# Kernel tuning notes

Measured on AMD Instinct MI355X. Metric: run time of the kernel, lower is better.

Reference implementation:

```python
import jax, jax.numpy as jnp
import numpy as np

B, N, T, ET = 256, 256, 100, 4
MSG_HID, MSG_OUT, N_HID, N_CLASSES = 128, 64, 64, 2
N_EDGES = N * (N - 1) // 2  # 32640


def _xavier(k, out_dim, in_dim):
    std = (2.0 / (in_dim + out_dim)) ** 0.5
    return jax.random.normal(k, (out_dim, in_dim), dtype=jnp.float32) * std


def setup_inputs() -> dict:
    key = jax.random.key(0)
    ks = jax.random.split(key, 7)
    return {
        "inputs": jax.random.normal(ks[0], (B, N, T), dtype=jnp.float32),
        "sparse_edges": jax.random.uniform(ks[1], (B, N_EDGES, ET), dtype=jnp.float32),
        "w1": _xavier(ks[2], MSG_HID, N), "b1": jnp.full((MSG_HID,), 0.1, jnp.float32),
        "w2": _xavier(ks[3], MSG_OUT, MSG_HID), "b2": jnp.full((MSG_OUT,), 0.1, jnp.float32),
        "wo1": _xavier(ks[4], N_HID, MSG_OUT), "bo1": jnp.full((N_HID,), 0.1, jnp.float32),
        "wo2": _xavier(ks[5], N_HID, N_HID), "bo2": jnp.full((N_HID,), 0.1, jnp.float32),
        "wo3": _xavier(ks[6], N_CLASSES, N_HID), "bo3": jnp.full((N_CLASSES,), 0.1, jnp.float32),
    }


def reference(inputs, sparse_edges, w1, b1, w2, b2, wo1, bo1, wo2, bo2, wo3, bo3):
    b, n, _ = inputs.shape
    r, c = np.triu_indices(n, k=1)  # static index pattern
    # Scatter all non-null edge types at once: [B, ET-1, N, N]
    se = jnp.swapaxes(sparse_edges[:, :, 1:], 1, 2)  # [B, ET-1, E]
    adj = jnp.zeros((b, se.shape[1], n, n), dtype=se.dtype)
    adj = adj.at[:, :, r, c].set(se)
    adj = adj + jnp.swapaxes(adj, -1, -2)  # symmetrize
    # Message MLP (dropout_prob = 0 -> identity)
    h = jax.nn.relu(jnp.einsum('beij,hj->beih', adj, w1) + b1)   # [B,ET-1,N,msg_hid]
    m = jax.nn.relu(jnp.einsum('beih,oh->beio', h, w2) + b2)     # [B,ET-1,N,msg_out]
    # Weighted sum over edge types: weight for type i is i*0.2, i=1..ET-1
    wts = (jnp.arange(1, sparse_edges.shape[2]) * 0.2).astype(m.dtype)
    out = jnp.einsum('beio,e->bio', m, wts)                      # [B,N,msg_out]
    # Output head
    p = jax.nn.relu(out @ wo1.T + bo1)
    p = jax.nn.relu(p @ wo2.T + bo2)
    p = jnp.mean(p, axis=1)  # mean over atoms
    return p @ wo3.T + bo3   # [B, n_classes]
```

## Files before the change

### kernel.cpp

```cpp
#include <hip/hip_runtime.h>

#define B_   256
#define N_   256
#define E_   32640
#define MH   128
#define MO   64
#define NH   64

typedef __bf16 bf16x8 __attribute__((ext_vector_type(8)));
typedef float  f32x4  __attribute__((ext_vector_type(4)));

__device__ __forceinline__ unsigned short cvt_bf16(float f) {
  unsigned u = __float_as_uint(f);
  u = (u + 0x7FFFu + ((u >> 16) & 1u)) >> 16;
  return (unsigned short)u;
}

__device__ __forceinline__ bf16x8 ldfrag(const unsigned short* base, int row, int kbyte, int rowbytes) {
  int byte = (row * rowbytes + kbyte) ^ ((row & 7) << 4);
  return *reinterpret_cast<const bf16x8*>(reinterpret_cast<const char*>(base) + byte);
}

__device__ __forceinline__ void st2(unsigned short* base, int row, int colbyte, int rowbytes, unsigned short v) {
  int byte = (row * rowbytes + colbyte) ^ ((row & 7) << 4);
  *reinterpret_cast<unsigned short*>(reinterpret_cast<char*>(base) + byte) = v;
}

__device__ __forceinline__ void stage_w(unsigned short* dst, const float* __restrict__ src,
                                        int elems, int lcols, int tid) {
  for (int t = tid; t < (elems >> 2); t += 512) {
    int idx = t << 2;
    const float4 v = *reinterpret_cast<const float4*>(src + idx);
    int row = idx >> lcols;
    ushort4 u = make_ushort4(cvt_bf16(v.x), cvt_bf16(v.y), cvt_bf16(v.z), cvt_bf16(v.w));
    int byte = (idx * 2) ^ ((row & 7) << 4);
    *reinterpret_cast<ushort4*>(reinterpret_cast<char*>(dst) + byte) = u;
  }
}

__global__ __launch_bounds__(512, 2) void mlpdec_kernel(
    const float* __restrict__ se_g,
    const float* __restrict__ w1,  const float* __restrict__ b1,
    const float* __restrict__ w2,  const float* __restrict__ b2,
    const float* __restrict__ wo1, const float* __restrict__ bo1,
    const float* __restrict__ wo2, const float* __restrict__ bo2,
    const float* __restrict__ wo3, const float* __restrict__ bo3,
    float* __restrict__ out)
{
  __shared__ __align__(16) unsigned short sW1[MH * N_];
  __shared__ __align__(16) unsigned short sW2[MO * MH];
  __shared__ __align__(16) unsigned short sWO1[NH * MO];
  __shared__ __align__(16) unsigned short sWO2[NH * NH];
  __shared__ __align__(16) unsigned short sA[3][32 * N_];
  __shared__ __align__(16) unsigned short sHXP[32 * MH];
  __shared__ float sB1[MH], sB2[MO], sBO1[NH], sBO2[NH], sWo3[2 * NH], sBo3[2];
  __shared__ float sAccW[8][64];
  __shared__ float sMean[64];

  const int tid = threadIdx.x;
  const int b   = blockIdx.x;
  const int w   = tid >> 6;
  const int l   = tid & 63;
  const int l15 = l & 15;
  const int lk  = l >> 4;
  const int kb0 = lk * 16;

  stage_w(sW1,  w1,  MH * N_, 8, tid);
  stage_w(sW2,  w2,  MO * MH, 7, tid);
  stage_w(sWO1, wo1, NH * MO, 6, tid);
  stage_w(sWO2, wo2, NH * NH, 6, tid);
  if (tid < 128) sB1[tid]  = b1[tid];
  if (tid < 64)  { sB2[tid] = b2[tid]; sBO1[tid] = bo1[tid]; sBO2[tid] = bo2[tid]; }
  if (tid < 128) sWo3[tid] = wo3[tid];
  if (tid < 2)   sBo3[tid] = bo3[tid];
  reinterpret_cast<float*>(sAccW)[tid] = 0.f;
  __syncthreads();

  const float4* seB = reinterpret_cast<const float4*>(se_g) + (size_t)b * E_;
  unsigned short* sH = sHXP;
  unsigned short* sX = sHXP;
  unsigned short* sP = sHXP + 32 * 64;

  const int tr  = w >> 2;
  const int tc2 = w & 3;
  const int tcB = (w & 3) * 2;

  for (int r0 = 0; r0 < N_; r0 += 32) {
    #pragma unroll
    for (int rr = 0; rr < 4; ++rr) {
      int lr = (w << 2) + rr;
      int gi = r0 + lr;
      int cnt = 255 - gi;
      int ubase = gi * 255 - ((gi * (gi - 1)) >> 1);
      for (int jj = l; jj < cnt; jj += 64) {
        float4 v = seB[ubase + jj];
        int cb = (gi + 1 + jj) * 2;
        st2(sA[0], lr, cb, 512, cvt_bf16(v.y));
        st2(sA[1], lr, cb, 512, cvt_bf16(v.z));
        st2(sA[2], lr, cb, 512, cvt_bf16(v.w));
      }
    }
    {
      int sub = tid >> 5, l32 = tid & 31;
      for (int j = sub; j < r0 + 31; j += 16) {
        int i0  = (j + 1 > r0) ? (j + 1) : r0;
        int cnt = r0 + 32 - i0;
        if (l32 < cnt) {
          int i = i0 + l32;
          int u = j * 255 - ((j * (j - 1)) >> 1) + (i - j - 1);
          float4 v = seB[u];
          int lr = i - r0, cb = j * 2;
          st2(sA[0], lr, cb, 512, cvt_bf16(v.y));
          st2(sA[1], lr, cb, 512, cvt_bf16(v.z));
          st2(sA[2], lr, cb, 512, cvt_bf16(v.w));
        }
      }
    }
    if (tid < 32) {
      int cb = (r0 + tid) * 2;
      st2(sA[0], tid, cb, 512, 0);
      st2(sA[1], tid, cb, 512, 0);
      st2(sA[2], tid, cb, 512, 0);
    }
    __syncthreads();

    f32x4 outAcc = {0.f, 0.f, 0.f, 0.f};

    for (int e = 0; e < 3; ++e) {
      {
        f32x4 acc0 = {0,0,0,0}, acc1 = {0,0,0,0};
        const unsigned short* sAe = sA[e];
        int arow  = tr * 16 + l15;
        int brow0 = (tcB + 0) * 16 + l15;
        int brow1 = (tcB + 1) * 16 + l15;
        #pragma unroll
        for (int ks = 0; ks < 8; ++ks) {
          int kb = ks * 64 + kb0;
          bf16x8 a   = ldfrag(sAe, arow,  kb, 512);
          bf16x8 bf0 = ldfrag(sW1, brow0, kb, 512);
          bf16x8 bf1 = ldfrag(sW1, brow1, kb, 512);
          acc0 = __builtin_amdgcn_mfma_f32_16x16x32_bf16(a, bf0, acc0, 0, 0, 0);
          acc1 = __builtin_amdgcn_mfma_f32_16x16x32_bf16(a, bf1, acc1, 0, 0, 0);
        }
        int   c0 = (tcB + 0) * 16 + l15, c1 = (tcB + 1) * 16 + l15;
        float bias0 = sB1[c0], bias1 = sB1[c1];
        #pragma unroll
        for (int r = 0; r < 4; ++r) {
          int hrow = tr * 16 + lk * 4 + r;
          st2(sH, hrow, c0 * 2, 256, cvt_bf16(fmaxf(acc0[r] + bias0, 0.f)));
          st2(sH, hrow, c1 * 2, 256, cvt_bf16(fmaxf(acc1[r] + bias1, 0.f)));
        }
      }
      __syncthreads();
      {
        f32x4 acc = {0,0,0,0};
        int arow = tr * 16 + l15;
        int brow = tc2 * 16 + l15;
        #pragma unroll
        for (int ks = 0; ks < 4; ++ks) {
          int kb = ks * 64 + kb0;
          bf16x8 a  = ldfrag(sH,  arow, kb, 256);
          bf16x8 bb = ldfrag(sW2, brow, kb, 256);
          acc = __builtin_amdgcn_mfma_f32_16x16x32_bf16(a, bb, acc, 0, 0, 0);
        }
        float bias = sB2[tc2 * 16 + l15];
        float wte  = 0.2f * (float)(e + 1);
        #pragma unroll
        for (int r = 0; r < 4; ++r)
          outAcc[r] += wte * fmaxf(acc[r] + bias, 0.f);
      }
      __syncthreads();
    }

    {
      int col = tc2 * 16 + l15;
      #pragma unroll
      for (int r = 0; r < 4; ++r) {
        int xr = tr * 16 + lk * 4 + r;
        st2(sX, xr, col * 2, 128, cvt_bf16(outAcc[r]));
      }
    }
    __syncthreads();
    {
      f32x4 acc = {0,0,0,0};
      int arow = tr * 16 + l15;
      int brow = tc2 * 16 + l15;
      #pragma unroll
      for (int ks = 0; ks < 2; ++ks) {
        int kb = ks * 64 + kb0;
        bf16x8 a  = ldfrag(sX,   arow, kb, 128);
        bf16x8 bb = ldfrag(sWO1, brow, kb, 128);
        acc = __builtin_amdgcn_mfma_f32_16x16x32_bf16(a, bb, acc, 0, 0, 0);
      }
      float bias = sBO1[tc2 * 16 + l15];
      #pragma unroll
      for (int r = 0; r < 4; ++r) {
        int pr = tr * 16 + lk * 4 + r;
        st2(sP, pr, (tc2 * 16 + l15) * 2, 128, cvt_bf16(fmaxf(acc[r] + bias, 0.f)));
      }
    }
    __syncthreads();
    {
      f32x4 acc = {0,0,0,0};
      int arow = tr * 16 + l15;
      int brow = tc2 * 16 + l15;
      #pragma unroll
      for (int ks = 0; ks < 2; ++ks) {
        int kb = ks * 64 + kb0;
        bf16x8 a  = ldfrag(sP,   arow, kb, 128);
        bf16x8 bb = ldfrag(sWO2, brow, kb, 128);
        acc = __builtin_amdgcn_mfma_f32_16x16x32_bf16(a, bb, acc, 0, 0, 0);
      }
      float bias = sBO2[tc2 * 16 + l15];
      float s = 0.f;
      #pragma unroll
      for (int r = 0; r < 4; ++r) s += fmaxf(acc[r] + bias, 0.f);
      s += __shfl_xor(s, 16);
      s += __shfl_xor(s, 32);
      if (lk == 0) sAccW[w][tc2 * 16 + l15] += s;
    }
    __syncthreads();
  }

  if (tid < 64) {
    float s = 0.f;
    #pragma unroll
    for (int ww = 0; ww < 8; ++ww) s += sAccW[ww][tid];
    sMean[tid] = s * (1.0f / 256.0f);
  }
  __syncthreads();
  if (tid < 128) {
    int c = tid >> 6;
    float v = sMean[l] * sWo3[c * 64 + l];
    #pragma unroll
    for (int off = 32; off > 0; off >>= 1) v += __shfl_down(v, off);
    if (l == 0) out[b * 2 + c] = v + sBo3[c];
  }
}

extern "C" void kernel_launch(void* const* d_in, const int* in_sizes, int n_in,
                              void* d_out, int out_size, void* d_ws, size_t ws_size,
                              hipStream_t stream) {
  (void)in_sizes; (void)n_in; (void)d_ws; (void)ws_size; (void)out_size;
  const float* se  = (const float*)d_in[1];
  const float* w1  = (const float*)d_in[2];
  const float* b1  = (const float*)d_in[3];
  const float* w2  = (const float*)d_in[4];
  const float* b2  = (const float*)d_in[5];
  const float* wo1 = (const float*)d_in[6];
  const float* bo1 = (const float*)d_in[7];
  const float* wo2 = (const float*)d_in[8];
  const float* bo2 = (const float*)d_in[9];
  const float* wo3 = (const float*)d_in[10];
  const float* bo3 = (const float*)d_in[11];
  mlpdec_kernel<<<dim3(256), dim3(512), 0, stream>>>(
      se, w1, b1, w2, b2, wo1, bo1, wo2, bo2, wo3, bo3, (float*)d_out);
}
```

Before: 105.4 us.

## Keep W1/W2 fragments in registers and process 64-row tiles with 1024 threads

Each wave now loads its W1 and W2 MFMA B-fragments once into registers as bf16, instead of staging the full W1 and W2 in LDS and re-reading them every k-step. The freed LDS holds a 64-row adjacency tile instead of a 32-row one, and the block grows to 1024 threads (16 waves). Each block therefore runs half as many outer iterations and barriers, and there are fewer LDS reads in the main GEMM. The cost is higher register pressure and per-wave duplicate global loads of the weight fragments.

```diff
diff --git a/kernel.cpp b/kernel.cpp
--- a/kernel.cpp
+++ b/kernel.cpp
@@ -1,14 +1,11 @@
 #include <hip/hip_runtime.h>
 
-#define B_   256
 #define N_   256
 #define E_   32640
-#define MH   128
-#define MO   64
-#define NH   64
 
 typedef __bf16 bf16x8 __attribute__((ext_vector_type(8)));
-typedef float  f32x4  __attribute__((ext_vector_type(4)));
+typedef unsigned short u16x8 __attribute__((ext_vector_type(8)));
+typedef float f32x4 __attribute__((ext_vector_type(4)));
 
 __device__ __forceinline__ unsigned short cvt_bf16(float f) {
   unsigned u = __float_as_uint(f);
@@ -26,19 +23,14 @@
   *reinterpret_cast<unsigned short*>(reinterpret_cast<char*>(base) + byte) = v;
 }
 
-__device__ __forceinline__ void stage_w(unsigned short* dst, const float* __restrict__ src,
-                                        int elems, int lcols, int tid) {
-  for (int t = tid; t < (elems >> 2); t += 512) {
-    int idx = t << 2;
-    const float4 v = *reinterpret_cast<const float4*>(src + idx);
-    int row = idx >> lcols;
-    ushort4 u = make_ushort4(cvt_bf16(v.x), cvt_bf16(v.y), cvt_bf16(v.z), cvt_bf16(v.w));
-    int byte = (idx * 2) ^ ((row & 7) << 4);
-    *reinterpret_cast<ushort4*>(reinterpret_cast<char*>(dst) + byte) = u;
-  }
-}
-
-__global__ __launch_bounds__(512, 2) void mlpdec_kernel(
+__device__ __forceinline__ bf16x8 pack8(float4 lo, float4 hi) {
+  u16x8 u;
+  u[0] = cvt_bf16(lo.x); u[1] = cvt_bf16(lo.y); u[2] = cvt_bf16(lo.z); u[3] = cvt_bf16(lo.w);
+  u[4] = cvt_bf16(hi.x); u[5] = cvt_bf16(hi.y); u[6] = cvt_bf16(hi.z); u[7] = cvt_bf16(hi.w);
+  return __builtin_bit_cast(bf16x8, u);
+}
+
+__global__ __launch_bounds__(1024, 4) void mlpdec_kernel(
     const float* __restrict__ se_g,
     const float* __restrict__ w1,  const float* __restrict__ b1,
     const float* __restrict__ w2,  const float* __restrict__ b2,
@@ -47,14 +39,12 @@
     const float* __restrict__ wo3, const float* __restrict__ bo3,
     float* __restrict__ out)
 {
-  __shared__ __align__(16) unsigned short sW1[MH * N_];
-  __shared__ __align__(16) unsigned short sW2[MO * MH];
-  __shared__ __align__(16) unsigned short sWO1[NH * MO];
-  __shared__ __align__(16) unsigned short sWO2[NH * NH];
-  __shared__ __align__(16) unsigned short sA[3][32 * N_];
-  __shared__ __align__(16) unsigned short sHXP[32 * MH];
-  __shared__ float sB1[MH], sB2[MO], sBO1[NH], sBO2[NH], sWo3[2 * NH], sBo3[2];
-  __shared__ float sAccW[8][64];
+  __shared__ __align__(16) unsigned short sA[3][64 * N_];
+  __shared__ __align__(16) unsigned short sH[64 * 128];
+  __shared__ __align__(16) unsigned short sWO1[64 * 64];
+  __shared__ __align__(16) unsigned short sWO2[64 * 64];
+  __shared__ float sB1[128], sB2[64], sBO1[64], sBO2[64], sWo3[128], sBo3[2];
+  __shared__ float sAccW[16][64];
   __shared__ float sMean[64];
 
   const int tid = threadIdx.x;
@@ -65,11 +55,51 @@
   const int lk  = l >> 4;
   const int kb0 = lk * 16;
 
-  stage_w(sW1,  w1,  MH * N_, 8, tid);
-  stage_w(sW2,  w2,  MO * MH, 7, tid);
-  stage_w(sWO1, wo1, NH * MO, 6, tid);
-  stage_w(sWO2, wo2, NH * NH, 6, tid);
-  if (tid < 128) sB1[tid]  = b1[tid];
+  const int c1 = w & 7;
+  const int rb = w >> 3;
+  const int c2 = w & 3;
+  const int r2 = w >> 2;
+
+  bf16x8 W1f[8];
+  {
+    const float* p = w1 + (c1 * 16 + l15) * 256 + lk * 8;
+    #pragma unroll
+    for (int ks = 0; ks < 8; ++ks) {
+      float4 lo = *reinterpret_cast<const float4*>(p + ks * 32);
+      float4 hi = *reinterpret_cast<const float4*>(p + ks * 32 + 4);
+      W1f[ks] = pack8(lo, hi);
+    }
+  }
+  bf16x8 W2f[4];
+  {
+    const float* p = w2 + (c2 * 16 + l15) * 128 + lk * 8;
+    #pragma unroll
+    for (int ks = 0; ks < 4; ++ks) {
+      float4 lo = *reinterpret_cast<const float4*>(p + ks * 32);
+      float4 hi = *reinterpret_cast<const float4*>(p + ks * 32 + 4);
+      W2f[ks] = pack8(lo, hi);
+    }
+  }
+
+  {
+    int t = tid;
+    int idx = t << 2;
+    {
+      const float4 v = *reinterpret_cast<const float4*>(wo1 + idx);
+      int row = idx >> 6;
+      ushort4 u = make_ushort4(cvt_bf16(v.x), cvt_bf16(v.y), cvt_bf16(v.z), cvt_bf16(v.w));
+      int byte = (idx * 2) ^ ((row & 7) << 4);
+      *reinterpret_cast<ushort4*>(reinterpret_cast<char*>(sWO1) + byte) = u;
+    }
+    {
+      const float4 v = *reinterpret_cast<const float4*>(wo2 + idx);
+      int row = idx >> 6;
+      ushort4 u = make_ushort4(cvt_bf16(v.x), cvt_bf16(v.y), cvt_bf16(v.z), cvt_bf16(v.w));
+      int byte = (idx * 2) ^ ((row & 7) << 4);
+      *reinterpret_cast<ushort4*>(reinterpret_cast<char*>(sWO2) + byte) = u;
+    }
+  }
+  if (tid < 128) sB1[tid] = b1[tid];
   if (tid < 64)  { sB2[tid] = b2[tid]; sBO1[tid] = bo1[tid]; sBO2[tid] = bo2[tid]; }
   if (tid < 128) sWo3[tid] = wo3[tid];
   if (tid < 2)   sBo3[tid] = bo3[tid];
@@ -77,15 +107,10 @@
   __syncthreads();
 
   const float4* seB = reinterpret_cast<const float4*>(se_g) + (size_t)b * E_;
-  unsigned short* sH = sHXP;
-  unsigned short* sX = sHXP;
-  unsigned short* sP = sHXP + 32 * 64;
-
-  const int tr  = w >> 2;
-  const int tc2 = w & 3;
-  const int tcB = (w & 3) * 2;
-
-  for (int r0 = 0; r0 < N_; r0 += 32) {
+  unsigned short* sX = sH;
+  unsigned short* sP = sH + 64 * 64;
+
+  for (int r0 = 0; r0 < N_; r0 += 64) {
     #pragma unroll
     for (int rr = 0; rr < 4; ++rr) {
       int lr = (w << 2) + rr;
@@ -100,23 +125,20 @@
         st2(sA[2], lr, cb, 512, cvt_bf16(v.w));
       }
     }
-    {
-      int sub = tid >> 5, l32 = tid & 31;
-      for (int j = sub; j < r0 + 31; j += 16) {
-        int i0  = (j + 1 > r0) ? (j + 1) : r0;
-        int cnt = r0 + 32 - i0;
-        if (l32 < cnt) {
-          int i = i0 + l32;
-          int u = j * 255 - ((j * (j - 1)) >> 1) + (i - j - 1);
-          float4 v = seB[u];
-          int lr = i - r0, cb = j * 2;
-          st2(sA[0], lr, cb, 512, cvt_bf16(v.y));
-          st2(sA[1], lr, cb, 512, cvt_bf16(v.z));
-          st2(sA[2], lr, cb, 512, cvt_bf16(v.w));
-        }
-      }
-    }
-    if (tid < 32) {
+    for (int j = w; j < r0 + 63; j += 16) {
+      int i0  = (j + 1 > r0) ? (j + 1) : r0;
+      int cnt = r0 + 64 - i0;
+      if (l < cnt) {
+        int i = i0 + l;
+        int u = j * 255 - ((j * (j - 1)) >> 1) + (i - j - 1);
+        float4 v = seB[u];
+        int lr = i - r0, cb = j * 2;
+        st2(sA[0], lr, cb, 512, cvt_bf16(v.y));
+        st2(sA[1], lr, cb, 512, cvt_bf16(v.z));
+        st2(sA[2], lr, cb, 512, cvt_bf16(v.w));
+      }
+    }
+    if (tid < 64) {
       int cb = (r0 + tid) * 2;
       st2(sA[0], tid, cb, 512, 0);
       st2(sA[1], tid, cb, 512, 0);
@@ -130,40 +152,34 @@
       {
         f32x4 acc0 = {0,0,0,0}, acc1 = {0,0,0,0};
         const unsigned short* sAe = sA[e];
-        int arow  = tr * 16 + l15;
-        int brow0 = (tcB + 0) * 16 + l15;
-        int brow1 = (tcB + 1) * 16 + l15;
+        int arow0 = rb * 16 + l15;
+        int arow1 = (rb + 2) * 16 + l15;
         #pragma unroll
         for (int ks = 0; ks < 8; ++ks) {
           int kb = ks * 64 + kb0;
-          bf16x8 a   = ldfrag(sAe, arow,  kb, 512);
-          bf16x8 bf0 = ldfrag(sW1, brow0, kb, 512);
-          bf16x8 bf1 = ldfrag(sW1, brow1, kb, 512);
-          acc0 = __builtin_amdgcn_mfma_f32_16x16x32_bf16(a, bf0, acc0, 0, 0, 0);
-          acc1 = __builtin_amdgcn_mfma_f32_16x16x32_bf16(a, bf1, acc1, 0, 0, 0);
+          bf16x8 a0 = ldfrag(sAe, arow0, kb, 512);
+          bf16x8 a1 = ldfrag(sAe, arow1, kb, 512);
+          acc0 = __builtin_amdgcn_mfma_f32_16x16x32_bf16(a0, W1f[ks], acc0, 0, 0, 0);
+          acc1 = __builtin_amdgcn_mfma_f32_16x16x32_bf16(a1, W1f[ks], acc1, 0, 0, 0);
         }
-        int   c0 = (tcB + 0) * 16 + l15, c1 = (tcB + 1) * 16 + l15;
-        float bias0 = sB1[c0], bias1 = sB1[c1];
+        int cc = c1 * 16 + l15;
+        float bias = sB1[cc];
         #pragma unroll
         for (int r = 0; r < 4; ++r) {
-          int hrow = tr * 16 + lk * 4 + r;
-          st2(sH, hrow, c0 * 2, 256, cvt_bf16(fmaxf(acc0[r] + bias0, 0.f)));
-          st2(sH, hrow, c1 * 2, 256, cvt_bf16(fmaxf(acc1[r] + bias1, 0.f)));
+          st2(sH, rb * 16 + lk * 4 + r,       cc * 2, 256, cvt_bf16(fmaxf(acc0[r] + bias, 0.f)));
+          st2(sH, (rb + 2) * 16 + lk * 4 + r, cc * 2, 256, cvt_bf16(fmaxf(acc1[r] + bias, 0.f)));
         }
       }
       __syncthreads();
       {
         f32x4 acc = {0,0,0,0};
-        int arow = tr * 16 + l15;
-        int brow = tc2 * 16 + l15;
+        int arow = r2 * 16 + l15;
         #pragma unroll
         for (int ks = 0; ks < 4; ++ks) {
-          int kb = ks * 64 + kb0;
-          bf16x8 a  = ldfrag(sH,  arow, kb, 256);
-          bf16x8 bb = ldfrag(sW2, brow, kb, 256);
-          acc = __builtin_amdgcn_mfma_f32_16x16x32_bf16(a, bb, acc, 0, 0, 0);
+          bf16x8 a = ldfrag(sH, arow, ks * 64 + kb0, 256);
+          acc = __builtin_amdgcn_mfma_f32_16x16x32_bf16(a, W2f[ks], acc, 0, 0, 0);
         }
-        float bias = sB2[tc2 * 16 + l15];
+        float bias = sB2[c2 * 16 + l15];
         float wte  = 0.2f * (float)(e + 1);
         #pragma unroll
         for (int r = 0; r < 4; ++r)
@@ -173,51 +189,45 @@
     }
 
     {
-      int col = tc2 * 16 + l15;
-      #pragma unroll
-      for (int r = 0; r < 4; ++r) {
-        int xr = tr * 16 + lk * 4 + r;
-        st2(sX, xr, col * 2, 128, cvt_bf16(outAcc[r]));
-      }
+      int col = c2 * 16 + l15;
+      #pragma unroll
+      for (int r = 0; r < 4; ++r)
+        st2(sX, r2 * 16 + lk * 4 + r, col * 2, 128, cvt_bf16(outAcc[r]));
     }
     __syncthreads();
     {
       f32x4 acc = {0,0,0,0};
-      int arow = tr * 16 + l15;
-      int brow = tc2 * 16 + l15;
+      int arow = r2 * 16 + l15;
+      int brow = c2 * 16 + l15;
       #pragma unroll
       for (int ks = 0; ks < 2; ++ks) {
-        int kb = ks * 64 + kb0;
-        bf16x8 a  = ldfrag(sX,   arow, kb, 128);
-        bf16x8 bb = ldfrag(sWO1, brow, kb, 128);
+        bf16x8 a  = ldfrag(sX,   arow, ks * 64 + kb0, 128);
+        bf16x8 bb = ldfrag(sWO1, brow, ks * 64 + kb0, 128);
         acc = __builtin_amdgcn_mfma_f32_16x16x32_bf16(a, bb, acc, 0, 0, 0);
       }
-      float bias = sBO1[tc2 * 16 + l15];
-      #pragma unroll
-      for (int r = 0; r < 4; ++r) {
-        int pr = tr * 16 + lk * 4 + r;
-        st2(sP, pr, (tc2 * 16 + l15) * 2, 128, cvt_bf16(fmaxf(acc[r] + bias, 0.f)));
-      }
+      float bias = sBO1[c2 * 16 + l15];
+      #pragma unroll
+      for (int r = 0; r < 4; ++r)
+        st2(sP, r2 * 16 + lk * 4 + r, (c2 * 16 + l15) * 2, 128, cvt_bf16(fmaxf(acc[r] + bias, 0.f)));
     }
     __syncthreads();
     {
       f32x4 acc = {0,0,0,0};
-      int arow = tr * 16 + l15;
-      int brow = tc2 * 16 + l15;
+      int arow = r2 * 16 + l15;
+      int brow = c2 * 16 + l15;
       #pragma unroll
       for (int ks = 0; ks < 2; ++ks) {
-        int kb = ks * 64 + kb0;
-        bf16x8 a  = ldfrag(sP,   arow, kb, 128);
-        bf16x8 bb = ldfrag(sWO2, brow, kb, 128);
+        bf16x8 a  = ldfrag(sP,   arow, ks * 64 + kb0, 128);
+        bf16x8 bb = ldfrag(sWO2, brow, ks * 64 + kb0, 128);
         acc = __builtin_amdgcn_mfma_f32_16x16x32_bf16(a, bb, acc, 0, 0, 0);
       }
-      float bias = sBO2[tc2 * 16 + l15];
+      float bias = sBO2[c2 * 16 + l15];
       float s = 0.f;
       #pragma unroll
       for (int r = 0; r < 4; ++r) s += fmaxf(acc[r] + bias, 0.f);
       s += __shfl_xor(s, 16);
       s += __shfl_xor(s, 32);
-      if (lk == 0) sAccW[w][tc2 * 16 + l15] += s;
+      if (lk == 0) sAccW[w][c2 * 16 + l15] += s;
     }
     __syncthreads();
   }
@@ -225,7 +235,7 @@
   if (tid < 64) {
     float s = 0.f;
     #pragma unroll
-    for (int ww = 0; ww < 8; ++ww) s += sAccW[ww][tid];
+    for (int ww = 0; ww < 16; ++ww) s += sAccW[ww][tid];
     sMean[tid] = s * (1.0f / 256.0f);
   }
   __syncthreads();
@@ -253,6 +263,6 @@
   const float* bo2 = (const float*)d_in[9];
   const float* wo3 = (const float*)d_in[10];
   const float* bo3 = (const float*)d_in[11];
-  mlpdec_kernel<<<dim3(256), dim3(512), 0, stream>>>(
+  mlpdec_kernel<<<dim3(256), dim3(1024), 0, stream>>>(
       se, w1, b1, w2, b2, wo1, bo1, wo2, bo2, wo3, bo3, (float*)d_out);
 }
```

Result: faster. 101.2 us (-4.0%).
